# Performance work log

Hardware: AMD Instinct MI355X
Metric: run time of the kernel (lower is better)

The kernel has to match this reference:

```python
import jax, jax.numpy as jnp
import numpy as np

B, T, S, U = 256, 64, 16, 4  # batch, channels, yt_img_size, upscale_factor


def setup_inputs() -> dict:
    key = jax.random.key(0)
    k1, k2, k3 = jax.random.split(key, 3)
    x = jax.random.normal(k1, (B, T, S, S), dtype=jnp.float32)
    # Stacked per-pixel Linear weights: (P pixels, out=U*U*T, in=T)
    W = jax.random.normal(k2, (S * S, U * U * T, T), dtype=jnp.float32) * 0.05
    b = jax.random.normal(k3, (S * S, U * U * T), dtype=jnp.float32) * 0.01
    return {"x": x, "W": W, "b": b}


def reference(x, W, b):
    Bn, Tn, Sn, _ = x.shape
    P = Sn * Sn
    Un = int(np.sqrt(W.shape[1] // Tn))  # upscale factor, static
    # Per-pixel grouped GEMM: each spatial location has its own Linear(T -> U*U*T)
    xp = x.reshape(Bn, Tn, P).transpose(2, 0, 1)          # (P, B, T)
    y = jnp.einsum('pbt,pot->pbo', xp, W) + b[:, None, :]  # (P, B, U*U*T)
    # Flat output per pixel is viewed as (T, U, U) and scattered to the (i*U:(i+1)*U, j*U:(j+1)*U) patch
    y = y.reshape(Sn, Sn, Bn, Tn, Un, Un)                  # (Si, Sj, B, T, Ui, Uj)
    y = y.transpose(2, 3, 0, 4, 1, 5)                      # (B, T, Si, Ui, Sj, Uj)
    return y.reshape(Bn, Tn, Sn * Un, Sn * Un)
```

## Files before the change

kernel.cpp:

```cpp
#include <hip/hip_runtime.h>
#include <hip/hip_bf16.h>


#define P_PIX 256
#define BATCH 256
#define KDIM 64
#define ODIM 1024
#define LDA 72

using bf16x8 = __attribute__((ext_vector_type(8))) short;
using f32x4  = __attribute__((ext_vector_type(4))) float;

__global__ __launch_bounds__(256) void transpose_convert(
    const float* __restrict__ x, __hip_bfloat16* __restrict__ xp)
{
    __shared__ float tile[64][65];
    const int R = BATCH * KDIM;
    int p0 = (blockIdx.x & 3) * 64;
    int r0 = (blockIdx.x >> 2) * 64;
    int tp = threadIdx.x & 63;
    int t4 = threadIdx.x >> 6;
    #pragma unroll
    for (int i = 0; i < 16; ++i) {
        int r = t4 + i * 4;
        tile[r][tp] = x[(size_t)(r0 + r) * P_PIX + p0 + tp];
    }
    __syncthreads();
    #pragma unroll
    for (int i = 0; i < 16; ++i) {
        int pl = t4 + i * 4;
        xp[(size_t)(p0 + pl) * R + r0 + tp] = __float2bfloat16(tile[tp][pl]);
    }
}

__global__ __launch_bounds__(256, 2) void gemm_pixel(
    const __hip_bfloat16* __restrict__ xp,
    const float* __restrict__ W,
    const float* __restrict__ bias,
    float* __restrict__ out)
{
    __shared__ __hip_bfloat16 As[128 * LDA];
    __shared__ __hip_bfloat16 Bs[128 * LDA];

    int g = blockIdx.x;
    int nt     = g & 7;
    int sjmod4 = (g >> 3) & 3;
    int q      = g >> 5;
    int mt  = q & 1;
    int sjg = (q >> 1) & 3;
    int si  = q >> 3;
    int p  = si * 16 + sjg * 4 + sjmod4;
    int m0 = mt * 128;
    int n0 = nt * 128;
    int tid = threadIdx.x;

    {
        const uint4* src = (const uint4*)(xp + (size_t)p * (BATCH * KDIM) + (size_t)m0 * KDIM);
        #pragma unroll
        for (int c = 0; c < 4; ++c) {
            int idx = c * 256 + tid;
            int row = idx >> 3, ch = idx & 7;
            uint4 v = src[idx];
            *(uint4*)(&As[row * LDA + ch * 8]) = v;
        }
    }
    {
        const float4* src = (const float4*)(W + (size_t)p * (ODIM * KDIM) + (size_t)n0 * KDIM);
        #pragma unroll
        for (int c = 0; c < 8; ++c) {
            int idx = c * 256 + tid;
            int row = idx >> 4, ch = idx & 15;
            float4 v = src[idx];
            __hip_bfloat16 h[4];
            h[0] = __float2bfloat16(v.x); h[1] = __float2bfloat16(v.y);
            h[2] = __float2bfloat16(v.z); h[3] = __float2bfloat16(v.w);
            *(uint2*)(&Bs[row * LDA + ch * 4]) = *(const uint2*)h;
        }
    }
    __syncthreads();

    int wave = tid >> 6;
    int lane = tid & 63;
    int wm = (wave & 1) * 64;
    int wn = (wave >> 1) * 64;
    int lrow = lane & 15;
    int quad = lane >> 4;

    f32x4 acc[4][4] = {};
    #pragma unroll
    for (int ks = 0; ks < 2; ++ks) {
        bf16x8 a[4], b[4];
        int kof = ks * 32 + quad * 8;
        #pragma unroll
        for (int i = 0; i < 4; ++i)
            a[i] = *(const bf16x8*)(&As[(wm + i * 16 + lrow) * LDA + kof]);
        #pragma unroll
        for (int i = 0; i < 4; ++i)
            b[i] = *(const bf16x8*)(&Bs[(wn + i * 16 + lrow) * LDA + kof]);
        #pragma unroll
        for (int i = 0; i < 4; ++i)
            #pragma unroll
            for (int j = 0; j < 4; ++j)
                acc[i][j] = __builtin_amdgcn_mfma_f32_16x16x32_bf16(a[i], b[j], acc[i][j], 0, 0, 0);
    }

    int sj = p & 15;
    #pragma unroll
    for (int j = 0; j < 4; ++j) {
        int o = n0 + wn + j * 16 + lrow;
        float bv = bias[(size_t)p * ODIM + o];
        int t = o >> 4, ui = (o >> 2) & 3, uj = o & 3;
        size_t base = ((size_t)t * 64 + si * 4 + ui) * 64 + sj * 4 + uj;
        #pragma unroll
        for (int i = 0; i < 4; ++i) {
            int brow = m0 + wm + i * 16 + quad * 4;
            #pragma unroll
            for (int r = 0; r < 4; ++r) {
                out[(size_t)(brow + r) * (64 * 64 * 64) + base] = acc[i][j][r] + bv;
            }
        }
    }
}

extern "C" void kernel_launch(void* const* d_in, const int* in_sizes, int n_in,
                              void* d_out, int out_size, void* d_ws, size_t ws_size,
                              hipStream_t stream) {
    const float* x    = (const float*)d_in[0];
    const float* W    = (const float*)d_in[1];
    const float* bias = (const float*)d_in[2];
    float* out = (float*)d_out;
    __hip_bfloat16* xp = (__hip_bfloat16*)d_ws;

    transpose_convert<<<1024, 256, 0, stream>>>(x, xp);
    gemm_pixel<<<4096, 256, 0, stream>>>(xp, W, bias, out);
}
```

Before: 479.5 us.

## Restructure pixel GEMM to swap operands and emit float4 output rows

Each block now covers one output channel t, one pixel row si and a 64-batch tile. Each wave handles four adjacent pixels and computes W·x^T, so that the accumulator lanes map directly to contiguous uj positions. Operands are loaded straight from global memory into registers with no shared-memory staging and no syncthreads. The epilogue writes float4 vectors, replacing the earlier scalar scattered stores into the strided output. The cost is that x tiles are reloaded per t block with no LDS reuse, and W rows are read in small 32-byte pieces per lane.

Result: slower. 526.4 us (+9.8%).

```diff
diff --git a/kernel.cpp b/kernel.cpp
--- a/kernel.cpp
+++ b/kernel.cpp
@@ -6,7 +6,6 @@
 #define BATCH 256
 #define KDIM 64
 #define ODIM 1024
-#define LDA 72
 
 using bf16x8 = __attribute__((ext_vector_type(8))) short;
 using f32x4  = __attribute__((ext_vector_type(4))) float;
@@ -39,85 +38,65 @@
     const float* __restrict__ bias,
     float* __restrict__ out)
 {
-    __shared__ __hip_bfloat16 As[128 * LDA];
-    __shared__ __hip_bfloat16 Bs[128 * LDA];
+    int g  = blockIdx.x;
+    int mt = g & 3;
+    int t  = (g >> 2) & 63;
+    int si = g >> 8;
 
-    int g = blockIdx.x;
-    int nt     = g & 7;
-    int sjmod4 = (g >> 3) & 3;
-    int q      = g >> 5;
-    int mt  = q & 1;
-    int sjg = (q >> 1) & 3;
-    int si  = q >> 3;
-    int p  = si * 16 + sjg * 4 + sjmod4;
-    int m0 = mt * 128;
-    int n0 = nt * 128;
-    int tid = threadIdx.x;
+    int tid  = threadIdx.x;
+    int w    = tid >> 6;
+    int lane = tid & 63;
+    int lrow = lane & 15;
+    int quad = lane >> 4;
+    int b0   = mt * 64;
 
-    {
-        const uint4* src = (const uint4*)(xp + (size_t)p * (BATCH * KDIM) + (size_t)m0 * KDIM);
+    f32x4 acc[4][4] = {};
+
+    #pragma unroll
+    for (int pp = 0; pp < 4; ++pp) {
+        int p = si * 16 + w * 4 + pp;
+
+        const float* wrow = W + ((size_t)p * ODIM + (size_t)t * 16 + lrow) * KDIM;
+        bf16x8 af[2];
         #pragma unroll
-        for (int c = 0; c < 4; ++c) {
-            int idx = c * 256 + tid;
-            int row = idx >> 3, ch = idx & 7;
-            uint4 v = src[idx];
-            *(uint4*)(&As[row * LDA + ch * 8]) = v;
+        for (int ks = 0; ks < 2; ++ks) {
+            float4 u0 = *(const float4*)(wrow + ks * 32 + quad * 8);
+            float4 u1 = *(const float4*)(wrow + ks * 32 + quad * 8 + 4);
+            __hip_bfloat16 h[8];
+            h[0] = __float2bfloat16(u0.x); h[1] = __float2bfloat16(u0.y);
+            h[2] = __float2bfloat16(u0.z); h[3] = __float2bfloat16(u0.w);
+            h[4] = __float2bfloat16(u1.x); h[5] = __float2bfloat16(u1.y);
+            h[6] = __float2bfloat16(u1.z); h[7] = __float2bfloat16(u1.w);
+            af[ks] = *(const bf16x8*)h;
+        }
+
+        const __hip_bfloat16* xbase = xp + (size_t)p * (BATCH * KDIM);
+        #pragma unroll
+        for (int j = 0; j < 4; ++j) {
+            const __hip_bfloat16* xrow = xbase + (size_t)(b0 + j * 16 + lrow) * KDIM;
+            #pragma unroll
+            for (int ks = 0; ks < 2; ++ks) {
+                bf16x8 bf = *(const bf16x8*)(xrow + ks * 32 + quad * 8);
+                acc[pp][j] = __builtin_amdgcn_mfma_f32_16x16x32_bf16(af[ks], bf, acc[pp][j], 0, 0, 0);
+            }
         }
     }
-    {
-        const float4* src = (const float4*)(W + (size_t)p * (ODIM * KDIM) + (size_t)n0 * KDIM);
+
+    #pragma unroll
+    for (int pp = 0; pp < 4; ++pp) {
+        int p  = si * 16 + w * 4 + pp;
+        int sj = w * 4 + pp;
+        float4 bv = *(const float4*)(bias + (size_t)p * ODIM + (size_t)t * 16 + quad * 4);
         #pragma unroll
-        for (int c = 0; c < 8; ++c) {
-            int idx = c * 256 + tid;
-            int row = idx >> 4, ch = idx & 15;
-            float4 v = src[idx];
-            __hip_bfloat16 h[4];
-            h[0] = __float2bfloat16(v.x); h[1] = __float2bfloat16(v.y);
-            h[2] = __float2bfloat16(v.z); h[3] = __float2bfloat16(v.w);
-            *(uint2*)(&Bs[row * LDA + ch * 4]) = *(const uint2*)h;
-        }
-    }
-    __syncthreads();
-
-    int wave = tid >> 6;
-    int lane = tid & 63;
-    int wm = (wave & 1) * 64;
-    int wn = (wave >> 1) * 64;
-    int lrow = lane & 15;
-    int quad = lane >> 4;
-
-    f32x4 acc[4][4] = {};
-    #pragma unroll
-    for (int ks = 0; ks < 2; ++ks) {
-        bf16x8 a[4], b[4];
-        int kof = ks * 32 + quad * 8;
-        #pragma unroll
-        for (int i = 0; i < 4; ++i)
-            a[i] = *(const bf16x8*)(&As[(wm + i * 16 + lrow) * LDA + kof]);
-        #pragma unroll
-        for (int i = 0; i < 4; ++i)
-            b[i] = *(const bf16x8*)(&Bs[(wn + i * 16 + lrow) * LDA + kof]);
-        #pragma unroll
-        for (int i = 0; i < 4; ++i)
-            #pragma unroll
-            for (int j = 0; j < 4; ++j)
-                acc[i][j] = __builtin_amdgcn_mfma_f32_16x16x32_bf16(a[i], b[j], acc[i][j], 0, 0, 0);
-    }
-
-    int sj = p & 15;
-    #pragma unroll
-    for (int j = 0; j < 4; ++j) {
-        int o = n0 + wn + j * 16 + lrow;
-        float bv = bias[(size_t)p * ODIM + o];
-        int t = o >> 4, ui = (o >> 2) & 3, uj = o & 3;
-        size_t base = ((size_t)t * 64 + si * 4 + ui) * 64 + sj * 4 + uj;
-        #pragma unroll
-        for (int i = 0; i < 4; ++i) {
-            int brow = m0 + wm + i * 16 + quad * 4;
-            #pragma unroll
-            for (int r = 0; r < 4; ++r) {
-                out[(size_t)(brow + r) * (64 * 64 * 64) + base] = acc[i][j][r] + bv;
-            }
+        for (int j = 0; j < 4; ++j) {
+            int b = b0 + j * 16 + lrow;
+            float4 v;
+            v.x = acc[pp][j][0] + bv.x;
+            v.y = acc[pp][j][1] + bv.y;
+            v.z = acc[pp][j][2] + bv.z;
+            v.w = acc[pp][j][3] + bv.w;
+            size_t off = ((((size_t)b * 64 + t) * 64) + si * 4 + quad) * 64 + sj * 4;
+            *(float4*)(out + off) = v;
         }
     }
 }
```
